# Kernel tuning notes

Measured on AMD Instinct MI355X. Metric: run time of the kernel, lower is better.

## Reference

```python
import jax, jax.numpy as jnp
import numpy as np
from jax import lax

L_STEPS = 10
MU = 0.1
GAUSS_KS = 51
GAUSS_SIGMA = 6.0
LEAKY_SLOPE = 0.01

# normalized sobel kernels (kornia normalized=True divides by sum(|k|)=8)
KX = jnp.array([[-1., 0., 1.], [-2., 0., 2.], [-1., 0., 1.]]) / 8.0
KY = KX.T


def _depthwise_valid(x, k2d):
    # x: [B,C,h,w] (already padded), k2d: [kh,kw]; cross-correlation per channel
    C = x.shape[1]
    kern = jnp.broadcast_to(k2d, (C, 1) + k2d.shape).astype(x.dtype)
    return lax.conv_general_dilated(x, kern, (1, 1), 'VALID',
                                    feature_group_count=C,
                                    dimension_numbers=('NCHW', 'OIHW', 'NCHW'))


def spatial_gradient(img):
    # img [B,1,h,w] -> [B,1,2,h,w] (dx, dy), replicate border like kornia
    p = jnp.pad(img, ((0, 0), (0, 0), (1, 1), (1, 1)), mode='edge')
    gx = _depthwise_valid(p, KX)
    gy = _depthwise_valid(p, KY)
    return jnp.stack([gx, gy], axis=2)


def _gauss1d(ks, sigma):
    x = jnp.arange(ks, dtype=jnp.float32) - (ks - 1) / 2.0
    g = jnp.exp(-0.5 * (x / sigma) ** 2)
    return g / jnp.sum(g)


def gaussian_blur(x):
    # border_type='constant' -> zero pad, separable depthwise blur
    g = _gauss1d(GAUSS_KS, GAUSS_SIGMA)
    p = GAUSS_KS // 2
    xp = jnp.pad(x, ((0, 0), (0, 0), (p, p), (p, p)))
    y = _depthwise_valid(xp, g[:, None])   # blur along H
    return _depthwise_valid(y, g[None, :])  # blur along W


def conv3x3(x, w, b=None):
    y = lax.conv_general_dilated(x, w, (1, 1), [(1, 1), (1, 1)],
                                 dimension_numbers=('NCHW', 'OIHW', 'NCHW'))
    if b is not None:
        y = y + b[None, :, None, None]
    return y


def res_block_apply(z, I, w1, b1, w2):
    x = jnp.concatenate([z, I], axis=1)          # [B,2,h,w]
    x = conv3x3(x, w1, b1)                        # [B,100,h,w]
    x = jnp.where(x > 0, x, LEAKY_SLOPE * x)
    return conv3x3(x, w2)                         # [B,1,h,w]


def deform_image(img, grid):
    # img [B,C,h,w], grid [B,h,w,2] pixel (x,y); bilinear with border clamp
    B, C, h, w = img.shape
    x, y = grid[..., 0], grid[..., 1]
    x0f, y0f = jnp.floor(x), jnp.floor(y)
    wx, wy = x - x0f, y - y0f
    x0 = jnp.clip(x0f.astype(jnp.int32), 0, w - 1)
    x1 = jnp.clip(x0f.astype(jnp.int32) + 1, 0, w - 1)
    y0 = jnp.clip(y0f.astype(jnp.int32), 0, h - 1)
    y1 = jnp.clip(y0f.astype(jnp.int32) + 1, 0, h - 1)
    bidx = jnp.arange(B)[:, None, None]
    Ia = img[bidx, :, y0, x0]  # [B,h,w,C]
    Ib = img[bidx, :, y0, x1]
    Ic = img[bidx, :, y1, x0]
    Id = img[bidx, :, y1, x1]
    wa = ((1 - wx) * (1 - wy))[..., None]
    wb = (wx * (1 - wy))[..., None]
    wc = ((1 - wx) * wy)[..., None]
    wd = (wx * wy)[..., None]
    out = wa * Ia + wb * Ib + wc * Ic + wd * Id
    return out.transpose(0, 3, 1, 2)


def _id_grid(h, w, dtype):
    xs = jnp.arange(w, dtype=dtype)
    ys = jnp.arange(h, dtype=dtype)
    gx, gy = jnp.meshgrid(xs, ys, indexing='xy')
    return jnp.stack([gx, gy], axis=-1)[None]  # [1,h,w,2] (x,y) pixel coords


def setup_inputs() -> dict:
    key = jax.random.key(0)
    ks = jax.random.split(key, 5)
    B, h, w = 4, 256, 256
    source = jax.random.normal(ks[0], (B, 1, h, w), jnp.float32)
    z0 = 0.1 * jax.random.normal(ks[1], (1, 1, h, w), jnp.float32)
    conv1_w = jax.random.normal(ks[2], (L_STEPS, 100, 2, 3, 3), jnp.float32) / np.sqrt(2 * 9)
    conv1_b = 0.01 * jax.random.normal(ks[3], (L_STEPS, 100), jnp.float32)
    conv2_w = jax.random.normal(ks[4], (L_STEPS, 1, 100, 3, 3), jnp.float32) / np.sqrt(100 * 9)
    return {"source": source, "z0": z0, "conv1_w": conv1_w,
            "conv1_b": conv1_b, "conv2_w": conv2_w}


def reference(source, z0, conv1_w, conv1_b, conv2_w):
    B, _, h, w = source.shape
    l = L_STEPS
    id_grid = _id_grid(h, w, source.dtype)
    z = jnp.broadcast_to(z0, (B,) + z0.shape[1:])
    images, residuals, fields, grads = [source], [z], [], []
    for i in range(l):
        g = spatial_gradient(images[i])                       # [B,1,2,h,w]
        grads.append(g)
        field = gaussian_blur(-residuals[i] * g[:, 0])        # [B,2,h,w]
        field = field.transpose(0, 2, 3, 1)                   # [B,h,w,2]
        fields.append(field)
        f = res_block_apply(residuals[i], images[i],
                            conv1_w[i], conv1_b[i], conv2_w[i]) / l
        z_next = residuals[i] + f
        residuals.append(z_next)
        deformation = id_grid - field / l
        images.append(deform_image(images[i], deformation)
                      + z_next * (MU ** 2) / l)
    return (jnp.stack(images), jnp.stack(fields),
            jnp.stack(residuals), jnp.stack(grads))
```

## Files before the change

kernel.cpp:

```cpp
#include <hip/hip_runtime.h>
#include <hip/hip_bf16.h>
#include <math.h>

#define B 4
#define H 256
#define W 256
#define HW 65536
#define BHW (B * HW)
#define LSTEPS 10
#define NCH 100
#define KS 51
#define KR 25

typedef __fp16 h2 __attribute__((ext_vector_type(2)));
typedef __fp16 half8 __attribute__((ext_vector_type(8)));
typedef float f32x4 __attribute__((ext_vector_type(4)));
typedef unsigned u32x4v __attribute__((ext_vector_type(4)));
typedef unsigned u32x2v __attribute__((ext_vector_type(2)));

static __device__ __forceinline__ h2 pack_f16(float a, float b) {
#if __has_builtin(__builtin_amdgcn_cvt_pkrtz)
    return __builtin_amdgcn_cvt_pkrtz(a, b);
#else
    h2 r; r.x = (__fp16)a; r.y = (__fp16)b; return r;
#endif
}
static __device__ __forceinline__ unsigned packu(float a, float b) {
    return __builtin_bit_cast(unsigned, pack_f16(a, b));
}

__global__ void init_kernel(const float* __restrict__ src, const float* __restrict__ z0,
                            const float* __restrict__ conv1_w, const float* __restrict__ conv1_b,
                            const float* __restrict__ conv2_w,
                            float* __restrict__ images0, float* __restrict__ res0,
                            unsigned* __restrict__ gwpk,
                            unsigned* __restrict__ a1, unsigned* __restrict__ a2) {
    int tid = blockIdx.x * 256 + threadIdx.x;
    images0[tid] = src[tid];
    res0[tid] = z0[tid & (HW - 1)];
    if (tid == 0) {
        float e[KS];
        float s = 0.f;
        for (int k = 0; k < KS; k++) {
            float x = (float)(k - KR) / 6.0f;
            e[k] = expf(-0.5f * x * x);
            s += e[k];
        }
        for (int k = 0; k < KS; k++) {
            float g = e[k] / s;
            gwpk[k] = packu(g, g);
        }
    }
    if (tid < LSTEPS * 112) {
        int i = tid / 112, c = tid % 112;
        unsigned* dst = a1 + (size_t)tid * 16;
        if (c < NCH) {
            const float* wz = conv1_w + ((size_t)i * NCH + c) * 18;
            float bias = conv1_b[(size_t)i * NCH + c];
#pragma unroll
            for (int t = 0; t < 9; t++) dst[t] = packu(wz[t], wz[9 + t]);
            dst[9] = packu(bias, 0.f);
#pragma unroll
            for (int t = 10; t < 16; t++) dst[t] = 0u;
        } else {
#pragma unroll
            for (int t = 0; t < 16; t++) dst[t] = 0u;
        }
    }
    if (tid >= 4096 && tid < 4096 + LSTEPS * 16) {
        int r = tid - 4096;
        int i = r / 16, q = r % 16;
        unsigned* dst = a2 + (size_t)r * 64;
        for (int cp = 0; cp < 64; cp++) {
            int c0 = 2 * cp, c1 = 2 * cp + 1;
            float f0 = (q < 9 && c0 < NCH) ? conv2_w[((size_t)i * NCH + c0) * 9 + q] : 0.f;
            float f1 = (q < 9 && c1 < NCH) ? conv2_w[((size_t)i * NCH + c1) * 9 + q] : 0.f;
            dst[cp] = packu(f0, f1);
        }
    }
}

__global__ __launch_bounds__(256, 4) void mfma_smap_kernel(
        const float* __restrict__ z, const float* __restrict__ img,
        const unsigned* __restrict__ a1, const unsigned* __restrict__ a2,
        __hip_bfloat16* __restrict__ S,
        float* __restrict__ grads_i, unsigned* __restrict__ t01) {
    __shared__ unsigned feat_l[256 * 16];
    __shared__ unsigned h_l[64 * 64];
    __shared__ float zrow[3][W + 2];
    __shared__ float irow[3][W + 2];
    int bid = blockIdx.x;
    int x8 = bid & 7;
    int t8 = bid >> 5;
    int j4 = (bid >> 3) & 3;
    int q8 = t8 * 8 + x8;
    int b = q8 >> 6;
    int y = (((q8 & 63) << 2) | j4);
    int x = threadIdx.x;
    int p = y * W + x;
    const float* zp = z + (b << 16);
    const float* ip = img + (b << 16);

    bool rv0, rv1, rv2;
#pragma unroll
    for (int r = 0; r < 3; r++) {
        int yy = y - 1 + r;
        bool rv = ((unsigned)yy < (unsigned)H);
        int yc = min(max(yy, 0), H - 1);
        zrow[r][x + 1] = rv ? zp[yc * W + x] : 0.f;
        irow[r][x + 1] = ip[yc * W + x];
        if (x == 0) {
            zrow[r][0] = 0.f;       zrow[r][W + 1] = 0.f;
            irow[r][0] = ip[yc * W + 0];
            irow[r][W + 1] = ip[yc * W + (W - 1)];
        }
        if (r == 0) rv0 = rv; else if (r == 1) rv1 = rv; else rv2 = rv;
    }
    __syncthreads();

    float ir[9], zv9[9];
#pragma unroll
    for (int r = 0; r < 3; r++)
#pragma unroll
        for (int c = 0; c < 3; c++) {
            ir[r * 3 + c] = irow[r][x + c];
            zv9[r * 3 + c] = zrow[r][x + c];
        }
    float gx = ((ir[2] + 2.f * ir[5] + ir[8]) - (ir[0] + 2.f * ir[3] + ir[6])) * 0.125f;
    float gy = ((ir[6] + 2.f * ir[7] + ir[8]) - (ir[0] + 2.f * ir[1] + ir[2])) * 0.125f;
    grads_i[(b * 2 + 0) * HW + p] = gx;
    grads_i[(b * 2 + 1) * HW + p] = gy;
    float zc = zv9[4];
    t01[(b << 16) + p] = packu(-zc * gx, -zc * gy);

    unsigned fd[16];
#pragma unroll
    for (int r = 0; r < 3; r++) {
        bool rv = (r == 0) ? rv0 : (r == 1) ? rv1 : rv2;
#pragma unroll
        for (int c = 0; c < 3; c++) {
            int k = r * 3 + c;
            bool ok = rv && ((unsigned)(x + c - 1) < (unsigned)W);
            float iv = ok ? ir[k] : 0.f;
            fd[k] = packu(zv9[k], iv);
        }
    }
    fd[9] = packu(1.0f, 0.f);
#pragma unroll
    for (int k = 10; k < 16; k++) fd[k] = 0u;

    {
        unsigned base = (unsigned)(x * 16);
        unsigned swzf = (unsigned)((x & 3) << 2);
#pragma unroll
        for (int g = 0; g < 4; g++) {
            u32x4v v = {fd[g * 4], fd[g * 4 + 1], fd[g * 4 + 2], fd[g * 4 + 3]};
            *(u32x4v*)(feat_l + base + ((unsigned)(g * 4) ^ swzf)) = v;
        }
    }
    if (x < 64) {
        unsigned swz0 = (unsigned)((x & 15) << 2);
        u32x4v zv = {0u, 0u, 0u, 0u};
        *(u32x4v*)(h_l + x * 64 + (56u ^ swz0)) = zv;
        *(u32x4v*)(h_l + x * 64 + (60u ^ swz0)) = zv;
    }

    int w = threadIdx.x >> 6;
    int lane = threadIdx.x & 63;
    int l15 = lane & 15, lg = lane >> 4;

    half8 A1f[7];
#pragma unroll
    for (int mt = 0; mt < 7; mt++)
        A1f[mt] = __builtin_bit_cast(half8,
            *(const u32x4v*)(a1 + (size_t)((mt * 16 + l15) * 16 + lg * 4)));
    half8 A2f[4];
#pragma unroll
    for (int ks = 0; ks < 4; ks++)
        A2f[ks] = __builtin_bit_cast(half8,
            *(const u32x4v*)(a2 + (size_t)(l15 * 64 + ks * 16 + lg * 4)));

    __syncthreads();

    unsigned hrow = (unsigned)((w * 16 + l15) * 64);
    unsigned swz = (unsigned)(l15 << 2);
    unsigned fswz = (unsigned)((l15 & 3) << 2);
    const h2 c001 = {(__fp16)0.01f, (__fp16)0.01f};

#pragma unroll
    for (int qt = 0; qt < 4; qt++) {
        int pxq = qt * 64 + w * 16;
        half8 B1f = __builtin_bit_cast(half8,
            *(const u32x4v*)(feat_l + (unsigned)((pxq + l15) * 16) + ((unsigned)(lg * 4) ^ fswz)));
        f32x4 zero4 = {0.f, 0.f, 0.f, 0.f};
        f32x4 acc[7];
#pragma unroll
        for (int mt = 0; mt < 7; mt++)
            acc[mt] = __builtin_amdgcn_mfma_f32_16x16x32_f16(A1f[mt], B1f, zero4, 0, 0, 0);
#pragma unroll
        for (int mt = 0; mt < 7; mt++) {
            h2 h01 = pack_f16(acc[mt][0], acc[mt][1]);
            h2 h23 = pack_f16(acc[mt][2], acc[mt][3]);
            h01 = __builtin_elementwise_max(h01, h01 * c001);
            h23 = __builtin_elementwise_max(h23, h23 * c001);
            u32x2v dv = {__builtin_bit_cast(unsigned, h01), __builtin_bit_cast(unsigned, h23)};
            unsigned c = (unsigned)(mt * 8 + lg * 2);
            *(u32x2v*)(h_l + hrow + (c ^ swz)) = dv;
        }
        f32x4 acc2 = {0.f, 0.f, 0.f, 0.f};
#pragma unroll
        for (int ks = 0; ks < 4; ks++) {
            half8 B2f = __builtin_bit_cast(half8,
                *(const u32x4v*)(h_l + hrow + ((unsigned)(ks * 16 + lg * 4) ^ swz)));
            acc2 = __builtin_amdgcn_mfma_f32_16x16x32_f16(A2f[ks], B2f, acc2, 0, 0, 0);
        }
        int xg = pxq + l15;
        size_t sbase = (size_t)(b << 16) + (size_t)y * W + xg;
#pragma unroll
        for (int r = 0; r < 4; r++) {
            int qq = lg * 4 + r;
            if (qq < 9) S[(size_t)qq * BHW + sbase] = __float2bfloat16(acc2[r]);
        }
    }
}

__global__ __launch_bounds__(1024, 1) void vhblur_deform_kernel(
        const unsigned* __restrict__ t01g,
        const unsigned* __restrict__ gwpk,
        float* __restrict__ fields_i,
        const float* __restrict__ img, const float* __restrict__ z,
        const __hip_bfloat16* __restrict__ S,
        float* __restrict__ res_next, float* __restrict__ img_next) {
    __shared__ unsigned st[54][W];
    __shared__ unsigned hs[4][W + 2 * KR];
    int bid = blockIdx.x;
    int b = bid >> 6;
    int y0 = (bid & 63) << 2;
    int tid = threadIdx.x;
    int r = tid >> 8;
    int x = tid & 255;
    const unsigned* t01 = t01g + (b << 16);

    for (int j = r; j < 54; j += 4) {
        int rr = y0 - KR + j;
        st[j][x] = ((unsigned)rr < (unsigned)H) ? t01[rr * W + x] : 0u;
    }
    __syncthreads();

    h2 vacc[3];
#pragma unroll
    for (int j = 0; j < 3; j++) { h2 zz = {(__fp16)0.f, (__fp16)0.f}; vacc[j] = zz; }
#pragma unroll
    for (int k = 0; k < KS; k++) {
        h2 tv = __builtin_bit_cast(h2, st[r + k][x]);
        h2 wv = __builtin_bit_cast(h2, gwpk[k]);
        vacc[k % 3] = wv * tv + vacc[k % 3];
    }
    h2 v01 = vacc[0] + vacc[1] + vacc[2];
    hs[r][KR + x] = __builtin_bit_cast(unsigned, v01);
    if (x < KR) hs[r][x] = 0u;
    else if (x >= W - KR) hs[r][x + 2 * KR] = 0u;
    __syncthreads();

    h2 hacc[3];
#pragma unroll
    for (int j = 0; j < 3; j++) { h2 zz = {(__fp16)0.f, (__fp16)0.f}; hacc[j] = zz; }
#pragma unroll
    for (int k = 0; k < KS; k++) {
        h2 sv = __builtin_bit_cast(h2, hs[r][x + k]);
        h2 wv = __builtin_bit_cast(h2, gwpk[k]);
        hacc[k % 3] = wv * sv + hacc[k % 3];
    }
    h2 a01 = hacc[0] + hacc[1] + hacc[2];
    float a0 = (float)a01.x, a1v = (float)a01.y;

    int y = y0 + r;
    int p = y * W + x;
    int gtid = (b << 16) + p;
    float2* fdst = (float2*)(fields_i + (size_t)gtid * 2);
    *fdst = make_float2(a0, a1v);

    float f = 0.f;
#pragma unroll
    for (int q = 0; q < 9; q++) {
        int yy = y - 1 + q / 3;
        int xx = x - 1 + q % 3;
        if (((unsigned)yy < (unsigned)H) && ((unsigned)xx < (unsigned)W))
            f += __bfloat162float(S[(size_t)q * BHW + (b << 16) + yy * W + xx]);
    }
    float zn = z[gtid] + f / 10.0f;
    res_next[gtid] = zn;

    float sx = (float)x - a0 / 10.0f;
    float sy = (float)y - a1v / 10.0f;
    float x0f = floorf(sx), y0f = floorf(sy);
    float wx = sx - x0f, wy = sy - y0f;
    int ix0 = min(max((int)x0f, 0), W - 1);
    int ix1 = min(max((int)x0f + 1, 0), W - 1);
    int iy0 = min(max((int)y0f, 0), H - 1);
    int iy1 = min(max((int)y0f + 1, 0), H - 1);
    const float* im = img + (b << 16);
    float Ia = im[iy0 * W + ix0], Ib = im[iy0 * W + ix1];
    float Ic = im[iy1 * W + ix0], Id = im[iy1 * W + ix1];
    float out = (1.f - wx) * (1.f - wy) * Ia + wx * (1.f - wy) * Ib
              + (1.f - wx) * wy * Ic + wx * wy * Id;
    img_next[gtid] = out + zn * 0.001f;
}

extern "C" void kernel_launch(void* const* d_in, const int* in_sizes, int n_in,
                              void* d_out, int out_size, void* d_ws, size_t ws_size,
                              hipStream_t stream) {
    const float* source  = (const float*)d_in[0];
    const float* z0      = (const float*)d_in[1];
    const float* conv1_w = (const float*)d_in[2];
    const float* conv1_b = (const float*)d_in[3];
    const float* conv2_w = (const float*)d_in[4];

    float* out = (float*)d_out;
    float* images    = out;
    float* fields    = images + (size_t)11 * B * HW;
    float* residuals = fields + (size_t)10 * B * HW * 2;
    float* grads     = residuals + (size_t)11 * B * HW;

    unsigned* t01 = (unsigned*)d_ws;
    __hip_bfloat16* S = (__hip_bfloat16*)(t01 + (size_t)BHW);
    unsigned* gwpk = (unsigned*)(S + (size_t)9 * BHW);
    unsigned* a1 = gwpk + 64;
    unsigned* a2 = a1 + (size_t)LSTEPS * 112 * 16;

    init_kernel<<<BHW / 256, 256, 0, stream>>>(source, z0, conv1_w, conv1_b, conv2_w,
                                               images, residuals, gwpk, a1, a2);

    for (int i = 0; i < LSTEPS; i++) {
        const float* img_i = images + (size_t)i * B * HW;
        const float* z_i   = residuals + (size_t)i * B * HW;
        float* fields_i    = fields + (size_t)i * B * HW * 2;

        mfma_smap_kernel<<<B * H, 256, 0, stream>>>(z_i, img_i,
                a1 + (size_t)i * 112 * 16, a2 + (size_t)i * 16 * 64, S,
                grads + (size_t)i * B * 2 * HW, t01);
        vhblur_deform_kernel<<<B * H / 4, 1024, 0, stream>>>(t01, gwpk, fields_i,
                img_i, z_i, S,
                residuals + (size_t)(i + 1) * B * HW, images + (size_t)(i + 1) * B * HW);
    }
}
```

Before: 230.1 us.

## Fuse blur/deform with next step's gradient and MFMA s-map kernel

Merges each step's blur+deform kernel with the next step's gradient/conv MFMA s-map computation into one launch. It computes a halo of two extra rows so the next image and residual tiles stay in LDS, and ping-pongs the t01 and S buffers between steps. This removes one kernel launch per step and the global round-trip of the new image and residual before the next step's convolutions. In exchange it recomputes the blur and deform for halo rows, uses a much larger LDS footprint, and drops the minimum-blocks launch bound.

After: 245.6 us. +6.7%, slower.

```diff
diff --git a/kernel.cpp b/kernel.cpp
--- a/kernel.cpp
+++ b/kernel.cpp
@@ -11,6 +11,15 @@
 #define NCH 100
 #define KS 51
 #define KR 25
+
+#define IMGN_OFF 0
+#define RESN_OFF 1548
+#define A_OFF    3096
+#define ST_OFF   A_OFF
+#define HS_OFF   (A_OFF + 14336)
+#define FEAT_OFF A_OFF
+#define HL_OFF   (A_OFF + 16384)
+#define LDS_DW   (A_OFF + 32768)
 
 typedef __fp16 h2 __attribute__((ext_vector_type(2)));
 typedef __fp16 half8 __attribute__((ext_vector_type(8)));
@@ -224,87 +233,226 @@
     }
 }
 
-__global__ __launch_bounds__(1024, 1) void vhblur_deform_kernel(
-        const unsigned* __restrict__ t01g,
+__global__ __launch_bounds__(1024) void fused_kernel(
+        const unsigned* __restrict__ t01_r, unsigned* __restrict__ t01_w,
+        const __hip_bfloat16* __restrict__ S_r, __hip_bfloat16* __restrict__ S_w,
         const unsigned* __restrict__ gwpk,
+        const unsigned* __restrict__ a1n, const unsigned* __restrict__ a2n,
         float* __restrict__ fields_i,
-        const float* __restrict__ img, const float* __restrict__ z,
-        const __hip_bfloat16* __restrict__ S,
-        float* __restrict__ res_next, float* __restrict__ img_next) {
-    __shared__ unsigned st[54][W];
-    __shared__ unsigned hs[4][W + 2 * KR];
-    int bid = blockIdx.x;
-    int b = bid >> 6;
-    int y0 = (bid & 63) << 2;
+        const float* __restrict__ img_i, const float* __restrict__ z_i,
+        float* __restrict__ res_next, float* __restrict__ img_next,
+        float* __restrict__ grads_next, int do_k1) {
+    __shared__ unsigned lds[LDS_DW];
+    float* imgn = (float*)(lds + IMGN_OFF);
+    float* resn = (float*)(lds + RESN_OFF);
+
+    int q = blockIdx.x;
+    int b = q >> 6;
+    int y0 = (q & 63) << 2;
     int tid = threadIdx.x;
     int r = tid >> 8;
     int x = tid & 255;
-    const unsigned* t01 = t01g + (b << 16);
-
-    for (int j = r; j < 54; j += 4) {
-        int rr = y0 - KR + j;
-        st[j][x] = ((unsigned)rr < (unsigned)H) ? t01[rr * W + x] : 0u;
-    }
-    __syncthreads();
-
-    h2 vacc[3];
-#pragma unroll
-    for (int j = 0; j < 3; j++) { h2 zz = {(__fp16)0.f, (__fp16)0.f}; vacc[j] = zz; }
-#pragma unroll
-    for (int k = 0; k < KS; k++) {
-        h2 tv = __builtin_bit_cast(h2, st[r + k][x]);
-        h2 wv = __builtin_bit_cast(h2, gwpk[k]);
-        vacc[k % 3] = wv * tv + vacc[k % 3];
-    }
-    h2 v01 = vacc[0] + vacc[1] + vacc[2];
-    hs[r][KR + x] = __builtin_bit_cast(unsigned, v01);
-    if (x < KR) hs[r][x] = 0u;
-    else if (x >= W - KR) hs[r][x + 2 * KR] = 0u;
-    __syncthreads();
-
-    h2 hacc[3];
-#pragma unroll
-    for (int j = 0; j < 3; j++) { h2 zz = {(__fp16)0.f, (__fp16)0.f}; hacc[j] = zz; }
-#pragma unroll
-    for (int k = 0; k < KS; k++) {
-        h2 sv = __builtin_bit_cast(h2, hs[r][x + k]);
-        h2 wv = __builtin_bit_cast(h2, gwpk[k]);
-        hacc[k % 3] = wv * sv + hacc[k % 3];
-    }
-    h2 a01 = hacc[0] + hacc[1] + hacc[2];
-    float a0 = (float)a01.x, a1v = (float)a01.y;
-
-    int y = y0 + r;
-    int p = y * W + x;
-    int gtid = (b << 16) + p;
-    float2* fdst = (float2*)(fields_i + (size_t)gtid * 2);
-    *fdst = make_float2(a0, a1v);
-
-    float f = 0.f;
-#pragma unroll
-    for (int q = 0; q < 9; q++) {
-        int yy = y - 1 + q / 3;
-        int xx = x - 1 + q % 3;
-        if (((unsigned)yy < (unsigned)H) && ((unsigned)xx < (unsigned)W))
-            f += __bfloat162float(S[(size_t)q * BHW + (b << 16) + yy * W + xx]);
-    }
-    float zn = z[gtid] + f / 10.0f;
-    res_next[gtid] = zn;
-
-    float sx = (float)x - a0 / 10.0f;
-    float sy = (float)y - a1v / 10.0f;
-    float x0f = floorf(sx), y0f = floorf(sy);
-    float wx = sx - x0f, wy = sy - y0f;
-    int ix0 = min(max((int)x0f, 0), W - 1);
-    int ix1 = min(max((int)x0f + 1, 0), W - 1);
-    int iy0 = min(max((int)y0f, 0), H - 1);
-    int iy1 = min(max((int)y0f + 1, 0), H - 1);
-    const float* im = img + (b << 16);
-    float Ia = im[iy0 * W + ix0], Ib = im[iy0 * W + ix1];
-    float Ic = im[iy1 * W + ix0], Id = im[iy1 * W + ix1];
-    float out = (1.f - wx) * (1.f - wy) * Ia + wx * (1.f - wy) * Ib
-              + (1.f - wx) * wy * Ic + wx * wy * Id;
-    img_next[gtid] = out + zn * 0.001f;
+    const unsigned* t01b = t01_r + (b << 16);
+
+    for (int j = r; j < 56; j += 4) {
+        int rr = y0 - 26 + j;
+        lds[ST_OFF + j * W + x] = ((unsigned)rr < (unsigned)H) ? t01b[rr * W + x] : 0u;
+    }
+    __syncthreads();
+    for (int j = r; j < 6; j += 4) {
+        h2 vacc[3];
+#pragma unroll
+        for (int t = 0; t < 3; t++) { h2 zz = {(__fp16)0.f, (__fp16)0.f}; vacc[t] = zz; }
+#pragma unroll
+        for (int k = 0; k < KS; k++) {
+            h2 tv = __builtin_bit_cast(h2, lds[ST_OFF + (j + k) * W + x]);
+            h2 wv = __builtin_bit_cast(h2, gwpk[k]);
+            vacc[k % 3] = wv * tv + vacc[k % 3];
+        }
+        h2 v01 = vacc[0] + vacc[1] + vacc[2];
+        lds[HS_OFF + j * 306 + KR + x] = __builtin_bit_cast(unsigned, v01);
+        if (x < KR) lds[HS_OFF + j * 306 + x] = 0u;
+        else if (x >= W - KR) lds[HS_OFF + j * 306 + x + 2 * KR] = 0u;
+    }
+    __syncthreads();
+    for (int j = r; j < 6; j += 4) {
+        int y = y0 - 1 + j;
+        if ((unsigned)y >= (unsigned)H) continue;
+        h2 hacc[3];
+#pragma unroll
+        for (int t = 0; t < 3; t++) { h2 zz = {(__fp16)0.f, (__fp16)0.f}; hacc[t] = zz; }
+#pragma unroll
+        for (int k = 0; k < KS; k++) {
+            h2 sv = __builtin_bit_cast(h2, lds[HS_OFF + j * 306 + x + k]);
+            h2 wv = __builtin_bit_cast(h2, gwpk[k]);
+            hacc[k % 3] = wv * sv + hacc[k % 3];
+        }
+        h2 a01 = hacc[0] + hacc[1] + hacc[2];
+        float a0 = (float)a01.x, a1v = (float)a01.y;
+
+        int p = y * W + x;
+        int gtid = (b << 16) + p;
+        float f = 0.f;
+#pragma unroll
+        for (int q9 = 0; q9 < 9; q9++) {
+            int yy = y - 1 + q9 / 3;
+            int xx = x - 1 + q9 % 3;
+            if (((unsigned)yy < (unsigned)H) && ((unsigned)xx < (unsigned)W))
+                f += __bfloat162float(S_r[(size_t)q9 * BHW + (b << 16) + yy * W + xx]);
+        }
+        float zn = z_i[gtid] + f / 10.0f;
+
+        float sx = (float)x - a0 / 10.0f;
+        float sy = (float)y - a1v / 10.0f;
+        float x0f = floorf(sx), y0f = floorf(sy);
+        float wx = sx - x0f, wy = sy - y0f;
+        int ix0 = min(max((int)x0f, 0), W - 1);
+        int ix1 = min(max((int)x0f + 1, 0), W - 1);
+        int iy0 = min(max((int)y0f, 0), H - 1);
+        int iy1 = min(max((int)y0f + 1, 0), H - 1);
+        const float* im = img_i + (b << 16);
+        float Ia = im[iy0 * W + ix0], Ib = im[iy0 * W + ix1];
+        float Ic = im[iy1 * W + ix0], Id = im[iy1 * W + ix1];
+        float out = (1.f - wx) * (1.f - wy) * Ia + wx * (1.f - wy) * Ib
+                  + (1.f - wx) * wy * Ic + wx * wy * Id;
+        float ivn = out + zn * 0.001f;
+
+        imgn[j * (W + 2) + x + 1] = ivn;
+        resn[j * (W + 2) + x + 1] = zn;
+        if (j >= 1 && j <= 4) {
+            float2* fdst = (float2*)(fields_i + (size_t)gtid * 2);
+            *fdst = make_float2(a0, a1v);
+            res_next[gtid] = zn;
+            img_next[gtid] = ivn;
+        }
+    }
+    __syncthreads();
+    if (!do_k1) return;
+
+    if (r == 0) {
+        if (y0 == 0)   { imgn[x + 1] = imgn[(W + 2) + x + 1]; resn[x + 1] = 0.f; }
+        if (y0 == 252) { imgn[5 * (W + 2) + x + 1] = imgn[4 * (W + 2) + x + 1];
+                         resn[5 * (W + 2) + x + 1] = 0.f; }
+    }
+    __syncthreads();
+    if (tid < 12) {
+        int j = tid >> 1, side = tid & 1;
+        if (side == 0) { imgn[j * (W + 2)] = imgn[j * (W + 2) + 1]; resn[j * (W + 2)] = 0.f; }
+        else { imgn[j * (W + 2) + W + 1] = imgn[j * (W + 2) + W]; resn[j * (W + 2) + W + 1] = 0.f; }
+    }
+    __syncthreads();
+
+    {
+        int y = y0 + r;
+        int p = y * W + x;
+        float ir[9], zv9[9];
+#pragma unroll
+        for (int dr = 0; dr < 3; dr++)
+#pragma unroll
+            for (int dc = 0; dc < 3; dc++) {
+                ir[dr * 3 + dc] = imgn[(r + dr) * (W + 2) + x + dc];
+                zv9[dr * 3 + dc] = resn[(r + dr) * (W + 2) + x + dc];
+            }
+        float gx = ((ir[2] + 2.f * ir[5] + ir[8]) - (ir[0] + 2.f * ir[3] + ir[6])) * 0.125f;
+        float gy = ((ir[6] + 2.f * ir[7] + ir[8]) - (ir[0] + 2.f * ir[1] + ir[2])) * 0.125f;
+        grads_next[(b * 2 + 0) * HW + p] = gx;
+        grads_next[(b * 2 + 1) * HW + p] = gy;
+        float zc = zv9[4];
+        t01_w[(b << 16) + p] = packu(-zc * gx, -zc * gy);
+
+        unsigned fd[16];
+#pragma unroll
+        for (int dr = 0; dr < 3; dr++) {
+            bool rv = ((unsigned)(y - 1 + dr) < (unsigned)H);
+#pragma unroll
+            for (int dc = 0; dc < 3; dc++) {
+                int k = dr * 3 + dc;
+                bool ok = rv && ((unsigned)(x + dc - 1) < (unsigned)W);
+                fd[k] = packu(zv9[k], ok ? ir[k] : 0.f);
+            }
+        }
+        fd[9] = packu(1.0f, 0.f);
+#pragma unroll
+        for (int k = 10; k < 16; k++) fd[k] = 0u;
+
+        unsigned* featr = lds + FEAT_OFF + r * 4096;
+        unsigned base = (unsigned)(x * 16);
+        unsigned swzf = (unsigned)((x & 3) << 2);
+#pragma unroll
+        for (int g = 0; g < 4; g++) {
+            u32x4v v = {fd[g * 4], fd[g * 4 + 1], fd[g * 4 + 2], fd[g * 4 + 3]};
+            *(u32x4v*)(featr + base + ((unsigned)(g * 4) ^ swzf)) = v;
+        }
+        if (x < 64) {
+            unsigned* hlr = lds + HL_OFF + r * 4096;
+            unsigned swz0 = (unsigned)((x & 15) << 2);
+            u32x4v zv = {0u, 0u, 0u, 0u};
+            *(u32x4v*)(hlr + x * 64 + (56u ^ swz0)) = zv;
+            *(u32x4v*)(hlr + x * 64 + (60u ^ swz0)) = zv;
+        }
+    }
+
+    int lane = tid & 63;
+    int l15 = lane & 15, lg = lane >> 4;
+    half8 A1f[7];
+#pragma unroll
+    for (int mt = 0; mt < 7; mt++)
+        A1f[mt] = __builtin_bit_cast(half8,
+            *(const u32x4v*)(a1n + (size_t)((mt * 16 + l15) * 16 + lg * 4)));
+    half8 A2f[4];
+#pragma unroll
+    for (int ks = 0; ks < 4; ks++)
+        A2f[ks] = __builtin_bit_cast(half8,
+            *(const u32x4v*)(a2n + (size_t)(l15 * 64 + ks * 16 + lg * 4)));
+
+    __syncthreads();
+
+    int w = tid >> 6;
+    int rl = w >> 2;
+    int w4 = w & 3;
+    unsigned* featr = lds + FEAT_OFF + rl * 4096;
+    unsigned* hlr = lds + HL_OFF + rl * 4096;
+    unsigned hrow = (unsigned)((w4 * 16 + l15) * 64);
+    unsigned swz = (unsigned)(l15 << 2);
+    unsigned fswz = (unsigned)((l15 & 3) << 2);
+    const h2 c001 = {(__fp16)0.01f, (__fp16)0.01f};
+    int yk = y0 + rl;
+
+#pragma unroll
+    for (int qt = 0; qt < 4; qt++) {
+        int pxq = qt * 64 + w4 * 16;
+        half8 B1f = __builtin_bit_cast(half8,
+            *(const u32x4v*)(featr + (unsigned)((pxq + l15) * 16) + ((unsigned)(lg * 4) ^ fswz)));
+        f32x4 zero4 = {0.f, 0.f, 0.f, 0.f};
+        f32x4 acc[7];
+#pragma unroll
+        for (int mt = 0; mt < 7; mt++)
+            acc[mt] = __builtin_amdgcn_mfma_f32_16x16x32_f16(A1f[mt], B1f, zero4, 0, 0, 0);
+#pragma unroll
+        for (int mt = 0; mt < 7; mt++) {
+            h2 h01 = pack_f16(acc[mt][0], acc[mt][1]);
+            h2 h23 = pack_f16(acc[mt][2], acc[mt][3]);
+            h01 = __builtin_elementwise_max(h01, h01 * c001);
+            h23 = __builtin_elementwise_max(h23, h23 * c001);
+            u32x2v dv = {__builtin_bit_cast(unsigned, h01), __builtin_bit_cast(unsigned, h23)};
+            unsigned c = (unsigned)(mt * 8 + lg * 2);
+            *(u32x2v*)(hlr + hrow + (c ^ swz)) = dv;
+        }
+        f32x4 acc2 = {0.f, 0.f, 0.f, 0.f};
+#pragma unroll
+        for (int ks = 0; ks < 4; ks++) {
+            half8 B2f = __builtin_bit_cast(half8,
+                *(const u32x4v*)(hlr + hrow + ((unsigned)(ks * 16 + lg * 4) ^ swz)));
+            acc2 = __builtin_amdgcn_mfma_f32_16x16x32_f16(A2f[ks], B2f, acc2, 0, 0, 0);
+        }
+        int xg = pxq + l15;
+        size_t sbase = (size_t)(b << 16) + (size_t)yk * W + xg;
+#pragma unroll
+        for (int rr = 0; rr < 4; rr++) {
+            int qq = lg * 4 + rr;
+            if (qq < 9) S_w[(size_t)qq * BHW + sbase] = __float2bfloat16(acc2[rr]);
+        }
+    }
 }
 
 extern "C" void kernel_launch(void* const* d_in, const int* in_sizes, int n_in,
@@ -322,25 +470,34 @@
     float* residuals = fields + (size_t)10 * B * HW * 2;
     float* grads     = residuals + (size_t)11 * B * HW;
 
-    unsigned* t01 = (unsigned*)d_ws;
-    __hip_bfloat16* S = (__hip_bfloat16*)(t01 + (size_t)BHW);
-    unsigned* gwpk = (unsigned*)(S + (size_t)9 * BHW);
+    unsigned* t01a = (unsigned*)d_ws;
+    unsigned* t01b = t01a + (size_t)BHW;
+    __hip_bfloat16* S0 = (__hip_bfloat16*)(t01b + (size_t)BHW);
+    __hip_bfloat16* S1 = S0 + (size_t)9 * BHW;
+    unsigned* gwpk = (unsigned*)(S1 + (size_t)9 * BHW);
     unsigned* a1 = gwpk + 64;
     unsigned* a2 = a1 + (size_t)LSTEPS * 112 * 16;
 
+    unsigned* t01buf[2] = {t01a, t01b};
+    __hip_bfloat16* Sbuf[2] = {S0, S1};
+
     init_kernel<<<BHW / 256, 256, 0, stream>>>(source, z0, conv1_w, conv1_b, conv2_w,
                                                images, residuals, gwpk, a1, a2);
+    mfma_smap_kernel<<<B * H, 256, 0, stream>>>(residuals, images, a1, a2, Sbuf[0],
+                                                grads, t01buf[0]);
 
     for (int i = 0; i < LSTEPS; i++) {
-        const float* img_i = images + (size_t)i * B * HW;
-        const float* z_i   = residuals + (size_t)i * B * HW;
-        float* fields_i    = fields + (size_t)i * B * HW * 2;
-
-        mfma_smap_kernel<<<B * H, 256, 0, stream>>>(z_i, img_i,
-                a1 + (size_t)i * 112 * 16, a2 + (size_t)i * 16 * 64, S,
-                grads + (size_t)i * B * 2 * HW, t01);
-        vhblur_deform_kernel<<<B * H / 4, 1024, 0, stream>>>(t01, gwpk, fields_i,
-                img_i, z_i, S,
-                residuals + (size_t)(i + 1) * B * HW, images + (size_t)(i + 1) * B * HW);
+        int rd = i & 1, wr = rd ^ 1;
+        int do_k1 = (i < LSTEPS - 1) ? 1 : 0;
+        const unsigned* a1n = do_k1 ? (a1 + (size_t)(i + 1) * 112 * 16) : a1;
+        const unsigned* a2n = do_k1 ? (a2 + (size_t)(i + 1) * 16 * 64) : a2;
+        float* gnext = do_k1 ? (grads + (size_t)(i + 1) * B * 2 * HW) : grads;
+
+        fused_kernel<<<256, 1024, 0, stream>>>(
+                t01buf[rd], t01buf[wr], Sbuf[rd], Sbuf[wr], gwpk, a1n, a2n,
+                fields + (size_t)i * B * HW * 2,
+                images + (size_t)i * B * HW, residuals + (size_t)i * B * HW,
+                residuals + (size_t)(i + 1) * B * HW, images + (size_t)(i + 1) * B * HW,
+                gnext, do_k1);
     }
 }
```
